# Kernel tuning notes

Hardware: AMD Instinct MI355X
Metric: run time of the kernel (lower is better)

Reference implementation:

```python
import jax, jax.numpy as jnp
import numpy as np

N, E, D, H, L, G, OUT = 16384, 65536, 64, 128, 3, 512, 128
EPS = 1e-5


def setup_inputs() -> dict:
    key = jax.random.key(0)
    ks = jax.random.split(key, 12)
    s = 0.05  # small init to keep res+ stack stable
    return {
        "x": jax.random.normal(ks[0], (N, D), jnp.float32),
        "edge_index": jax.random.randint(ks[1], (2, E), 0, N, jnp.int32),
        "edge_attr": jax.random.normal(ks[2], (E, D), jnp.float32),
        "batch": jnp.sort(jax.random.randint(ks[3], (N,), 0, G, jnp.int32)),
        # per-layer params, stacked on leading layer dim L
        "ln_scale": jnp.ones((L, D), jnp.float32),
        "ln_bias": jnp.zeros((L, D), jnp.float32),
        "W1": jax.random.normal(ks[4], (L, D, H), jnp.float32) * s,
        "b1": jnp.zeros((L, H), jnp.float32),
        "W2": jax.random.normal(ks[5], (L, H, D * D), jnp.float32) * s,
        "b2": jnp.zeros((L, D * D), jnp.float32),
        "root": jax.random.normal(ks[6], (L, D, D), jnp.float32) * s,
        "conv_b": jnp.zeros((L, D), jnp.float32),
        # head params
        "dense_W": jax.random.normal(ks[7], (D, D), jnp.float32) * s,
        "dense_b": jnp.zeros((D,), jnp.float32),
        "out_W": jax.random.normal(ks[8], (D, OUT), jnp.float32) * s,
        "out_b": jnp.zeros((OUT,), jnp.float32),
    }


def _layer_norm(h, scale, bias):
    mu = jnp.mean(h, axis=-1, keepdims=True)
    var = jnp.mean((h - mu) ** 2, axis=-1, keepdims=True)
    return (h - mu) * jax.lax.rsqrt(var + EPS) * scale + bias


def _gnn_layer(x, edge_index, edge_attr, ln_scale, ln_bias, W1, b1, W2, b2, root, conv_b):
    # DeepGCNLayer block='res+': h = conv(dropout(act(norm(x)))); return x + h
    # (dropout is identity in eval/reference)
    h = jax.nn.leaky_relu(_layer_norm(x, ln_scale, ln_bias))
    src, dst = edge_index[0], edge_index[1]
    # NNConv: per-edge DxD weight from edge MLP (MapE2NxN with LeakyReLU)
    w = jax.nn.leaky_relu(edge_attr @ W1 + b1) @ W2 + b2       # [E, D*D]
    w = w.reshape(-1, D, D)                                     # [E, D, D]
    msg = jnp.einsum('ed,edf->ef', h[src], w)                   # [E, D]
    num = jax.ops.segment_sum(msg, dst, num_segments=N)         # [N, D]
    deg = jax.ops.segment_sum(jnp.ones((msg.shape[0],), msg.dtype), dst, num_segments=N)
    agg = num / jnp.maximum(deg, 1.0)[:, None]                  # mean aggregation
    conv = agg + h @ root + conv_b                              # root weight + bias
    return x + conv


def reference(x, edge_index, edge_attr, batch, ln_scale, ln_bias, W1, b1, W2, b2,
              root, conv_b, dense_W, dense_b, out_W, out_b):
    for l in range(L):
        x = _gnn_layer(x, edge_index, edge_attr, ln_scale[l], ln_bias[l],
                       W1[l], b1[l], W2[l], b2[l], root[l], conv_b[l])
    x = x @ dense_W + dense_b
    # global_mean_pool over graphs
    num = jax.ops.segment_sum(x, batch, num_segments=G)
    cnt = jax.ops.segment_sum(jnp.ones((x.shape[0],), x.dtype), batch, num_segments=G)
    pooled = num / jnp.maximum(cnt, 1.0)[:, None]
    pooled = jax.nn.leaky_relu(pooled)
    return pooled @ out_W + out_b
```

## Files before the change

kernel.cpp:

```cpp
#include <hip/hip_runtime.h>
#include <hip/hip_bf16.h>

#define NN 16384
#define EE 65536
#define DD 64
#define HH 128
#define LL 3
#define GG 512
#define OUTD 128
#define NEG 0.01f

#define CHUNK 8192
#define KSEG 8


typedef __attribute__((ext_vector_type(8))) short short8;
typedef __attribute__((ext_vector_type(4))) float f32x4;

__device__ __forceinline__ float leaky(float x){ return x > 0.f ? x : NEG * x; }
__device__ __forceinline__ unsigned short f2bf(float f){
  union { float f; unsigned int u; } v; v.f = f;
  unsigned int r = v.u + 0x7fffu + ((v.u >> 16) & 1u);
  return (unsigned short)(r >> 16);
}

#define CV_A (EE*DD)
#define CV_B (LL*HH*DD)
#define CV_C (LL*64*8192)
#define PRE0 (NN/4)
#define PRE1 ((CV_A+CV_B+CV_C)/256)
#define PRE2 (EE/256)

__global__ void k_pre(const float* x_in, const float* ln_s, const float* ln_b,
                      float* x_cur, float* h, int* deg, int* cursor, int* cnt, float* pooled,
                      const float* ea, const float* W1, const float* W2,
                      unsigned short* eab, unsigned short* W1T, unsigned short* W2T,
                      const int* ei, const int* batch){
  int t = threadIdx.x;
  int b = blockIdx.x;
  if (b < PRE0){
    int i = b*256 + t;
    if (i < NN){ deg[i] = 0; cursor[i] = 0; }
    if (i < GG) cnt[i] = 0;
    if (i < GG*DD) pooled[i] = 0.f;
    int lane = t & 63, nl = t >> 6;
    int n = b*4 + nl;
    float v = x_in[(size_t)n*DD + lane];
    x_cur[(size_t)n*DD + lane] = v;
    float s = v;
    for (int m=1;m<64;m<<=1) s += __shfl_xor(s, m, 64);
    float mu = s * (1.0f/64.0f);
    float dv = v - mu;
    float q = dv*dv;
    for (int m=1;m<64;m<<=1) q += __shfl_xor(q, m, 64);
    float var = q * (1.0f/64.0f);
    float w = dv * rsqrtf(var + 1e-5f) * ln_s[lane] + ln_b[lane];
    h[(size_t)n*DD + lane] = leaky(w);
    return;
  }
  if (b < PRE0 + PRE1){
    int idx = (b - PRE0)*256 + t;
    if (idx < CV_A){
      eab[idx] = f2bf(ea[idx]);
    } else if (idx < CV_A + CV_B){
      int i = idx - CV_A;
      int l = i >> 13, r = i & 8191;
      int j = r >> 6, d = r & 63;
      W1T[i] = f2bf(W1[(size_t)l*DD*HH + d*HH + j]);
    } else {
      int i = idx - CV_A - CV_B;
      int l = i >> 19, rem = i & ((1<<19)-1);
      int f = rem >> 13, c = rem & 8191;
      int kk = c & 1, j = (c>>1) & 3, lane = (c>>3) & 63, ii = (c>>9) & 7, q = (c>>12) & 1;
      int idxu = 2*lane + kk;
      int d = 32*q + 4*ii + j;
      int kd = idxu*64 + d;
      W2T[i] = f2bf(W2[(size_t)l*HH*DD*DD + (size_t)kd*DD + f]);
    }
    return;
  }
  {
    int e = (b - PRE0 - PRE1)*256 + t;
    atomicAdd(&deg[ei[EE + e]], 1);
    if (e < NN) atomicAdd(&cnt[batch[e]], 1);
  }
}

__global__ void k_scan(const int* deg, int* row_ptr){
  __shared__ int part[256];
  int t = threadIdx.x;
  int base = t*64; int s = 0;
  for (int i=0;i<64;++i) s += deg[base+i];
  part[t] = s; __syncthreads();
  for (int off=1; off<256; off<<=1){
    int v = (t>=off)?part[t-off]:0; __syncthreads();
    part[t] += v; __syncthreads();
  }
  int run = (t==0)?0:part[t-1];
  if (t==0) row_ptr[0] = 0;
  for (int i=0;i<64;++i){ run += deg[base+i]; row_ptr[base+i+1] = run; }
}
__global__ void k_fill(const int* ei, const int* row_ptr, int* cursor,
                       int* edge_id, int* src_sorted){
  int e = blockIdx.x*256 + threadIdx.x;
  if (e < EE){
    int d = ei[EE + e];
    int pos = row_ptr[d] + atomicAdd(&cursor[d], 1);
    edge_id[pos] = e;
    src_sorted[pos] = ei[e];
  }
}

__global__ __launch_bounds__(256, 2)
void k_mlp3(const unsigned short* eab, const unsigned short* W1T, const float* b1,
            const int* edge_id, unsigned short* ug){
  __shared__ __align__(16) unsigned short a_lds[128][72];
  __shared__ __align__(16) unsigned short b_lds[128][72];
  __shared__ __align__(16) unsigned short c_lds[128][136];
  int t = threadIdx.x;
  int l  = blockIdx.x >> 9;
  int e0 = (blockIdx.x & 511) * 128;
  {
    int row = t >> 1, col = (t & 1) * 32;
    int eid = edge_id[e0 + row];
    const float4* sa = (const float4*)(eab + (size_t)eid*DD + col);
    const float4* sb = (const float4*)(W1T + (size_t)l*HH*DD + (size_t)row*DD + col);
    #pragma unroll
    for (int i=0;i<4;++i){
      *(float4*)&a_lds[row][col + 8*i] = sa[i];
      *(float4*)&b_lds[row][col + 8*i] = sb[i];
    }
  }
  __syncthreads();
  int wave = t >> 6, lane = t & 63;
  int m0 = (wave >> 1) * 64, j0 = (wave & 1) * 64;
  int lr = lane & 15, lq = lane >> 4;
  f32x4 acc[4][4];
  #pragma unroll
  for (int a=0;a<4;++a)
    #pragma unroll
    for (int b=0;b<4;++b) acc[a][b] = (f32x4){0.f,0.f,0.f,0.f};
  #pragma unroll
  for (int ks=0; ks<2; ++ks){
    short8 av[4];
    #pragma unroll
    for (int mt=0; mt<4; ++mt) av[mt] = *(const short8*)&a_lds[m0 + mt*16 + lr][ks*32 + lq*8];
    #pragma unroll
    for (int jt=0; jt<4; ++jt){
      short8 bv = *(const short8*)&b_lds[j0 + jt*16 + lr][ks*32 + lq*8];
      #pragma unroll
      for (int mt=0; mt<4; ++mt)
        acc[mt][jt] = __builtin_amdgcn_mfma_f32_16x16x32_bf16(av[mt], bv, acc[mt][jt], 0, 0, 0);
    }
  }
  #pragma unroll
  for (int mt=0; mt<4; ++mt)
    #pragma unroll
    for (int jt=0; jt<4; ++jt){
      int col = j0 + jt*16 + lr;
      float bj = b1[l*HH + col];
      #pragma unroll
      for (int r=0; r<4; ++r){
        int row = m0 + mt*16 + lq*4 + r;
        c_lds[row][col] = f2bf(leaky(acc[mt][jt][r] + bj));
      }
    }
  __syncthreads();
  {
    int row = t >> 1, half = t & 1;
    float4* dst = (float4*)(ug + (size_t)l*EE*HH + (size_t)(e0 + row)*HH + half*64);
    #pragma unroll
    for (int i=0;i<8;++i) dst[i] = *(const float4*)&c_lds[row][half*64 + 8*i];
  }
}

__global__ __launch_bounds__(256, 4)
void k_sbuild5(const unsigned short* ug, const float* h, const int* row_ptr,
               const int* src_sorted,
               unsigned short* S, float* Hs, int chunk_base){
  int t = threadIdx.x, wave = t >> 6, lane = t & 63;
  int q = wave & 1;
  int nloc = blockIdx.x*2 + (wave >> 1);
  int n = chunk_base + nloc;
  int r0 = row_ptr[n], r1 = row_ptr[n+1];
  int dbase = 32*q;
  int lhalf = lane & 31;
  const unsigned int* ugd = (const unsigned int*)ug;
  float acc[64];
  #pragma unroll
  for (int i=0;i<64;++i) acc[i] = 0.f;
  float hs = 0.f;
  int pos = r0;
  for (; pos + 4 <= r1; pos += 4){
    int sa0 = src_sorted[pos],   sb0 = src_sorted[pos+1];
    int sa1 = src_sorted[pos+2], sb1 = src_sorted[pos+3];
    int sel0 = (lane < 32) ? sa0 : sb0;
    int sel1 = (lane < 32) ? sa1 : sb1;
    float hv0 = h[(size_t)sel0*DD + dbase + lhalf];
    float hv1 = h[(size_t)sel1*DD + dbase + lhalf];
    unsigned int ua0 = ugd[(size_t)(pos+0)*64 + lane];
    unsigned int ub0 = ugd[(size_t)(pos+1)*64 + lane];
    unsigned int ua1 = ugd[(size_t)(pos+2)*64 + lane];
    unsigned int ub1 = ugd[(size_t)(pos+3)*64 + lane];
    hs += hv0 + hv1;
    int h0 = __float_as_int(hv0), h1 = __float_as_int(hv1);
    float ua0l = __uint_as_float(ua0 << 16), ua0h = __uint_as_float(ua0 & 0xFFFF0000u);
    float ub0l = __uint_as_float(ub0 << 16), ub0h = __uint_as_float(ub0 & 0xFFFF0000u);
    float ua1l = __uint_as_float(ua1 << 16), ua1h = __uint_as_float(ua1 & 0xFFFF0000u);
    float ub1l = __uint_as_float(ub1 << 16), ub1h = __uint_as_float(ub1 & 0xFFFF0000u);
    #pragma unroll
    for (int dd=0; dd<32; ++dd){
      float sa_ = __int_as_float(__builtin_amdgcn_readlane(h0, dd));
      float sb_ = __int_as_float(__builtin_amdgcn_readlane(h0, 32+dd));
      float sa2 = __int_as_float(__builtin_amdgcn_readlane(h1, dd));
      float sb2 = __int_as_float(__builtin_amdgcn_readlane(h1, 32+dd));
      acc[dd*2+0] += ua0l*sa_; acc[dd*2+1] += ua0h*sa_;
      acc[dd*2+0] += ub0l*sb_; acc[dd*2+1] += ub0h*sb_;
      acc[dd*2+0] += ua1l*sa2; acc[dd*2+1] += ua1h*sa2;
      acc[dd*2+0] += ub1l*sb2; acc[dd*2+1] += ub1h*sb2;
    }
  }
  for (; pos + 2 <= r1; pos += 2){
    int sa = src_sorted[pos], sb = src_sorted[pos+1];
    int sel = (lane < 32) ? sa : sb;
    float hv = h[(size_t)sel*DD + dbase + lhalf];
    unsigned int ua = ugd[(size_t)(pos+0)*64 + lane];
    unsigned int ub = ugd[(size_t)(pos+1)*64 + lane];
    hs += hv;
    int h0 = __float_as_int(hv);
    float ual = __uint_as_float(ua << 16), uah = __uint_as_float(ua & 0xFFFF0000u);
    float ubl = __uint_as_float(ub << 16), ubh = __uint_as_float(ub & 0xFFFF0000u);
    #pragma unroll
    for (int dd=0; dd<32; ++dd){
      float sa_ = __int_as_float(__builtin_amdgcn_readlane(h0, dd));
      float sb_ = __int_as_float(__builtin_amdgcn_readlane(h0, 32+dd));
      acc[dd*2+0] += ual*sa_; acc[dd*2+1] += uah*sa_;
      acc[dd*2+0] += ubl*sb_; acc[dd*2+1] += ubh*sb_;
    }
  }
  if (pos < r1){
    int s = src_sorted[pos];
    float hv = h[(size_t)s*DD + dbase + lhalf];
    unsigned int ua = ugd[(size_t)pos*64 + lane];
    hs += (lane < 32) ? hv : 0.f;
    int h0 = __float_as_int(hv);
    float ual = __uint_as_float(ua << 16), uah = __uint_as_float(ua & 0xFFFF0000u);
    #pragma unroll
    for (int dd=0; dd<32; ++dd){
      float sa_ = __int_as_float(__builtin_amdgcn_readlane(h0, dd));
      acc[dd*2+0] += ual*sa_; acc[dd*2+1] += uah*sa_;
    }
  }
  float4* Srow4 = (float4*)(S + (size_t)nloc*8192);
  #pragma unroll
  for (int i=0;i<8;++i){
    union { unsigned int u[4]; float4 v; } b;
    #pragma unroll
    for (int j=0;j<4;++j){
      int dd = 4*i + j;
      b.u[j] = (unsigned int)f2bf(acc[dd*2+0]) | ((unsigned int)f2bf(acc[dd*2+1]) << 16);
    }
    Srow4[(q*8 + i)*64 + lane] = b.v;
  }
  float hs2 = hs + __shfl_xor(hs, 32, 64);
  if (lane < 32) Hs[(size_t)n*DD + dbase + lane] = hs2;
}

__global__ __launch_bounds__(256, 2)
void k_gemm(const unsigned short* S, const unsigned short* W2T,
            float* num_part, int chunk_base){
  __shared__ __align__(16) unsigned short a_lds[128][136];
  __shared__ __align__(16) unsigned short b_lds[64][136];
  int t = threadIdx.x;
  int wave = t >> 6, lane = t & 63;
  int rowblk = blockIdx.x, kseg = blockIdx.y;
  int lr = lane & 15, lq = lane >> 4;
  f32x4 acc[2][4];
  #pragma unroll
  for (int a=0;a<2;++a)
    #pragma unroll
    for (int b=0;b<4;++b) acc[a][b] = (f32x4){0.f,0.f,0.f,0.f};
  int m0 = wave * 32;
  int ra = t >> 1, qa = t & 1;
  int rb = t >> 2, qb = t & 3;
  for (int it = 0; it < 8; ++it){
    int kbase = kseg*1024 + it*128;
    {
      const float4* sa = (const float4*)(S + (size_t)(rowblk*128 + ra)*8192 + kbase + qa*64);
      float4* da = (float4*)&a_lds[ra][qa*64];
      #pragma unroll
      for (int i=0;i<8;++i) da[i] = sa[i];
      const float4* sb = (const float4*)(W2T + (size_t)rb*8192 + kbase + qb*32);
      float4* db = (float4*)&b_lds[rb][qb*32];
      #pragma unroll
      for (int i=0;i<4;++i) db[i] = sb[i];
    }
    __syncthreads();
    #pragma unroll
    for (int kk=0; kk<128; kk+=32){
      short8 a0 = *(const short8*)&a_lds[m0 + lr][kk + lq*8];
      short8 a1 = *(const short8*)&a_lds[m0 + 16 + lr][kk + lq*8];
      #pragma unroll
      for (int ft=0; ft<4; ++ft){
        short8 bv = *(const short8*)&b_lds[ft*16 + lr][kk + lq*8];
        acc[0][ft] = __builtin_amdgcn_mfma_f32_16x16x32_bf16(a0, bv, acc[0][ft], 0, 0, 0);
        acc[1][ft] = __builtin_amdgcn_mfma_f32_16x16x32_bf16(a1, bv, acc[1][ft], 0, 0, 0);
      }
    }
    __syncthreads();
  }
  float* dstp = num_part + (size_t)kseg*NN*DD;
  #pragma unroll
  for (int rt=0; rt<2; ++rt)
    #pragma unroll
    for (int ft=0; ft<4; ++ft)
      #pragma unroll
      for (int rr=0; rr<4; ++rr){
        int m = m0 + rt*16 + lq*4 + rr;
        int f = ft*16 + lr;
        int n = chunk_base + rowblk*128 + m;
        dstp[(size_t)n*DD + f] = acc[rt][ft][rr];
      }
}

__global__ void k_update_ln(float* x, const float* num_part, float* h, const float* Hs,
                            const int* deg, const float* root, const float* b2,
                            const float* conv_b, const float* ln_s, const float* ln_b,
                            int l, int do_ln){
  __shared__ float rl[64][64];
  __shared__ float b2l[64][64];
  __shared__ float hrow[4][64];
  __shared__ float hsrow[4][64];
  int t = threadIdx.x;
  int f = t & 63, nl = t >> 6;
  for (int idx=t; idx<4096; idx+=256){
    rl[idx>>6][idx&63]  = root[(size_t)l*4096 + idx];
    b2l[idx>>6][idx&63] = b2[(size_t)l*4096 + idx];
  }
  int nbase = blockIdx.x*16;
  float cb = conv_b[l*DD + f];
  for (int i=0;i<4;++i){
    int n = nbase + i*4 + nl;
    __syncthreads();
    hrow[nl][f]  = h[(size_t)n*DD + f];
    hsrow[nl][f] = Hs[(size_t)n*DD + f];
    __syncthreads();
    float dg = (float)deg[n]; if (dg < 1.f) dg = 1.f;
    float nsum = 0.f;
    #pragma unroll
    for (int p=0; p<KSEG; ++p) nsum += num_part[(size_t)p*NN*DD + (size_t)n*DD + f];
    float acc = x[(size_t)n*DD + f] + nsum/dg + cb;
    #pragma unroll
    for (int d=0; d<64; ++d)
      acc += hrow[nl][d]*rl[d][f] + hsrow[nl][d]*b2l[d][f];
    x[(size_t)n*DD + f] = acc;
    if (do_ln){
      int lp = l + 1;
      float s = acc;
      for (int m=1;m<64;m<<=1) s += __shfl_xor(s, m, 64);
      float mu = s * (1.0f/64.0f);
      float dv = acc - mu;
      float qv = dv*dv;
      for (int m=1;m<64;m<<=1) qv += __shfl_xor(qv, m, 64);
      float var = qv * (1.0f/64.0f);
      float w = dv * rsqrtf(var + 1e-5f) * ln_s[lp*DD + f] + ln_b[lp*DD + f];
      h[(size_t)n*DD + f] = leaky(w);
    }
  }
}

__global__ void k_dense_pool(const float* x, const float* dW, const float* db,
                             const int* batch, float* pooled){
  __shared__ float wl[64][64];
  __shared__ float xrow[4][64];
  int t = threadIdx.x;
  int f = t & 63, nl = t >> 6;
  for (int idx=t; idx<4096; idx+=256) wl[idx>>6][idx&63] = dW[idx];
  int nbase = blockIdx.x*16;
  float dbf = db[f];
  for (int i=0;i<4;++i){
    int n = nbase + i*4 + nl;
    __syncthreads();
    xrow[nl][f] = x[(size_t)n*DD + f];
    __syncthreads();
    float acc = dbf;
    #pragma unroll
    for (int d=0; d<64; ++d) acc += xrow[nl][d]*wl[d][f];
    atomicAdd(&pooled[(size_t)batch[n]*DD + f], acc);
  }
}

__global__ void k_final(const float* pooled, const int* cnt, const float* oW,
                        const float* ob, float* out){
  __shared__ float p[64];
  int g = blockIdx.x, t = threadIdx.x;
  if (t < 64){
    float c = (float)cnt[g]; if (c < 1.f) c = 1.f;
    p[t] = leaky(pooled[(size_t)g*DD + t] / c);
  }
  __syncthreads();
  float acc = ob[t];
  #pragma unroll
  for (int f=0; f<64; ++f) acc += p[f]*oW[(size_t)f*OUTD + t];
  out[(size_t)g*OUTD + t] = acc;
}

__global__ void k_diag(float* out, float val, int n){
  int i = blockIdx.x*256 + threadIdx.x;
  if (i < n) out[i] = (i==0) ? val : 0.f;
}

extern "C" void kernel_launch(void* const* d_in, const int* in_sizes, int n_in,
                              void* d_out, int out_size, void* d_ws, size_t ws_size,
                              hipStream_t stream){
  const float* x_in  = (const float*)d_in[0];
  const int*   ei    = (const int*)d_in[1];
  const float* ea    = (const float*)d_in[2];
  const int*   batch = (const int*)d_in[3];
  const float* ln_s  = (const float*)d_in[4];
  const float* ln_b  = (const float*)d_in[5];
  const float* W1    = (const float*)d_in[6];
  const float* b1    = (const float*)d_in[7];
  const float* W2    = (const float*)d_in[8];
  const float* b2    = (const float*)d_in[9];
  const float* root  = (const float*)d_in[10];
  const float* convb = (const float*)d_in[11];
  const float* dW    = (const float*)d_in[12];
  const float* db    = (const float*)d_in[13];
  const float* oW    = (const float*)d_in[14];
  const float* ob    = (const float*)d_in[15];
  float* out = (float*)d_out;

  char* ws = (char*)d_ws;
  size_t off = 0;
  auto alloc = [&](size_t bytes)->char*{
    char* p = ws + off; off = (off + bytes + 255) & ~(size_t)255; return p;
  };
  float* x_cur  = (float*)alloc((size_t)NN*DD*4);
  float* h      = (float*)alloc((size_t)NN*DD*4);
  unsigned short* ug  = (unsigned short*)alloc((size_t)LL*EE*HH*2);
  float* num_part = (float*)alloc((size_t)KSEG*NN*DD*4);
  float* Hs     = (float*)alloc((size_t)NN*DD*4);
  unsigned short* S   = (unsigned short*)alloc((size_t)CHUNK*8192*2);
  unsigned short* W2T = (unsigned short*)alloc((size_t)LL*8192*64*2);
  unsigned short* eab = (unsigned short*)alloc((size_t)EE*DD*2);
  unsigned short* W1T = (unsigned short*)alloc((size_t)LL*HH*DD*2);
  int* deg     = (int*)alloc((size_t)NN*4);
  int* row_ptr = (int*)alloc((size_t)(NN+1)*4);
  int* cursor  = (int*)alloc((size_t)NN*4);
  int* edge_id = (int*)alloc((size_t)EE*4);
  int* src_sorted = (int*)alloc((size_t)EE*4);
  int* cnt     = (int*)alloc((size_t)GG*4);
  float* pooled= (float*)alloc((size_t)GG*DD*4);
  size_t needed = off;
  if (ws_size < needed){
    k_diag<<<(out_size+255)/256, 256, 0, stream>>>(out, (float)ws_size, out_size);
    return;
  }

  k_pre <<<PRE0+PRE1+PRE2, 256, 0, stream>>>(x_in, ln_s, ln_b, x_cur, h, deg, cursor, cnt,
                                             pooled, ea, W1, W2, eab, W1T, W2T, ei, batch);
  k_scan<<<1, 256, 0, stream>>>(deg, row_ptr);
  k_fill<<<EE/256, 256, 0, stream>>>(ei, row_ptr, cursor, edge_id, src_sorted);
  k_mlp3<<<LL*(EE/128), 256, 0, stream>>>(eab, W1T, b1, edge_id, ug);

  for (int l=0; l<LL; ++l){
    const unsigned short* ugl = ug + (size_t)l*EE*HH;
    for (int c=0; c<NN/CHUNK; ++c){
      k_sbuild5<<<CHUNK/2, 256, 0, stream>>>(ugl, h, row_ptr, src_sorted, S, Hs, c*CHUNK);
      k_gemm   <<<dim3(CHUNK/128, KSEG), 256, 0, stream>>>(S, W2T + (size_t)l*8192*64, num_part, c*CHUNK);
    }
    k_update_ln<<<NN/16, 256, 0, stream>>>(x_cur, num_part, h, Hs, deg, root, b2, convb,
                                           ln_s, ln_b, l, (l < LL-1) ? 1 : 0);
  }
  k_dense_pool<<<NN/16, 256, 0, stream>>>(x_cur, dW, db, batch, pooled);
  k_final     <<<GG, 128, 0, stream>>>(pooled, cnt, oW, ob, out);
}
```

Baseline: 592.0 us.

## Fuse per-node S construction with W2 GEMM in shared memory

Replaces the two-kernel pipeline (build the per-node S matrix in global memory, then a split-K GEMM writing partial sums) with one fused kernel. Each block of 32 nodes builds K-slices of S in swizzled LDS and immediately multiplies them by W2T with MFMA, accumulating over all K in registers. This removes the large global S buffer and the KSEG partial-sum reduction, and W2T is re-laid out to match. In exchange, each node re-reads its edge gather once per K-slice (8 times), and the grid is smaller with a heavy LDS footprint, which can limit occupancy.

```diff
diff --git a/kernel.cpp b/kernel.cpp
--- a/kernel.cpp
+++ b/kernel.cpp
@@ -9,9 +9,6 @@
 #define GG 512
 #define OUTD 128
 #define NEG 0.01f
-
-#define CHUNK 8192
-#define KSEG 8
 
 
 typedef __attribute__((ext_vector_type(8))) short short8;
@@ -71,11 +68,10 @@
       int i = idx - CV_A - CV_B;
       int l = i >> 19, rem = i & ((1<<19)-1);
       int f = rem >> 13, c = rem & 8191;
-      int kk = c & 1, j = (c>>1) & 3, lane = (c>>3) & 63, ii = (c>>9) & 7, q = (c>>12) & 1;
-      int idxu = 2*lane + kk;
-      int d = 32*q + 4*ii + j;
-      int kd = idxu*64 + d;
-      W2T[i] = f2bf(W2[(size_t)l*HH*DD*DD + (size_t)kd*DD + f]);
+      int ks = c >> 10, cl = c & 1023;
+      int d = cl >> 4, il = cl & 15;
+      int kh = ks*16 + il;
+      W2T[i] = f2bf(W2[(size_t)l*HH*DD*DD + (size_t)kh*DD*DD + (size_t)d*DD + f]);
     }
     return;
   }
@@ -174,156 +170,102 @@
   }
 }
 
-__global__ __launch_bounds__(256, 4)
-void k_sbuild5(const unsigned short* ug, const float* h, const int* row_ptr,
-               const int* src_sorted,
-               unsigned short* S, float* Hs, int chunk_base){
+#define ACC2(w, hv, base) { \
+  float lo_ = __uint_as_float((w) << 16); \
+  float hi_ = __uint_as_float((w) & 0xffff0000u); \
+  acc[(base)]   += lo_*(hv); \
+  acc[(base)+1] += hi_*(hv); }
+
+#define EDGE_ACC(aa, bb, hv) \
+  ACC2((aa).x, hv, 0)  ACC2((aa).y, hv, 2)  ACC2((aa).z, hv, 4)  ACC2((aa).w, hv, 6) \
+  ACC2((bb).x, hv, 8)  ACC2((bb).y, hv,10)  ACC2((bb).z, hv,12)  ACC2((bb).w, hv,14)
+
+__global__ __launch_bounds__(256)
+void k_fused(const unsigned short* ug, const float* h, const int* row_ptr,
+             const int* src_sorted, const unsigned short* W2T,
+             float* num, float* Hs){
+  __shared__ __align__(16) unsigned short Sm[32*1024];
+  char* Sb = (char*)Sm;
   int t = threadIdx.x, wave = t >> 6, lane = t & 63;
-  int q = wave & 1;
-  int nloc = blockIdx.x*2 + (wave >> 1);
-  int n = chunk_base + nloc;
-  int r0 = row_ptr[n], r1 = row_ptr[n+1];
-  int dbase = 32*q;
-  int lhalf = lane & 31;
-  const unsigned int* ugd = (const unsigned int*)ug;
-  float acc[64];
+  int g0 = blockIdx.x * 32;
+  int lr = lane & 15, lq = lane >> 4;
+  int f0 = wave * 16;
+  f32x4 acc0 = (f32x4){0.f,0.f,0.f,0.f};
+  f32x4 acc1 = (f32x4){0.f,0.f,0.f,0.f};
+  int wbase = (wave*8)*2048 + lane*32;
+
+  for (int ks = 0; ks < 8; ++ks){
+    const unsigned short* ugk = ug + ks*16;
+    for (int ni = 0; ni < 8; ++ni){
+      int n = g0 + wave*8 + ni;
+      int r0 = row_ptr[n], r1 = row_ptr[n+1];
+      float acc[16];
+      #pragma unroll
+      for (int i=0;i<16;++i) acc[i] = 0.f;
+      float hs = 0.f;
+      int pos = r0;
+      for (; pos + 4 <= r1; pos += 4){
+        int s0 = src_sorted[pos+0], s1 = src_sorted[pos+1];
+        int s2 = src_sorted[pos+2], s3 = src_sorted[pos+3];
+        const uint4* u0 = (const uint4*)(ugk + (size_t)(pos+0)*HH);
+        const uint4* u1 = (const uint4*)(ugk + (size_t)(pos+1)*HH);
+        const uint4* u2 = (const uint4*)(ugk + (size_t)(pos+2)*HH);
+        const uint4* u3 = (const uint4*)(ugk + (size_t)(pos+3)*HH);
+        float hv0 = h[(size_t)s0*DD + lane];
+        float hv1 = h[(size_t)s1*DD + lane];
+        float hv2 = h[(size_t)s2*DD + lane];
+        float hv3 = h[(size_t)s3*DD + lane];
+        uint4 a0 = u0[0], c0 = u0[1];
+        uint4 a1 = u1[0], c1 = u1[1];
+        uint4 a2 = u2[0], c2 = u2[1];
+        uint4 a3 = u3[0], c3 = u3[1];
+        hs += (hv0 + hv1) + (hv2 + hv3);
+        EDGE_ACC(a0, c0, hv0)
+        EDGE_ACC(a1, c1, hv1)
+        EDGE_ACC(a2, c2, hv2)
+        EDGE_ACC(a3, c3, hv3)
+      }
+      for (; pos < r1; ++pos){
+        int s0 = src_sorted[pos];
+        const uint4* u0 = (const uint4*)(ugk + (size_t)pos*HH);
+        float hv0 = h[(size_t)s0*DD + lane];
+        uint4 a0 = u0[0], c0 = u0[1];
+        hs += hv0;
+        EDGE_ACC(a0, c0, hv0)
+      }
+      unsigned int w[8];
+      #pragma unroll
+      for (int i=0;i<8;++i)
+        w[i] = (unsigned int)f2bf(acc[2*i]) | ((unsigned int)f2bf(acc[2*i+1]) << 16);
+      int nloc = wave*8 + ni;
+      int off = (wbase + ni*2048) ^ ((nloc & 7) << 4);
+      *(float4*)(Sb + off)        = *(const float4*)&w[0];
+      *(float4*)(Sb + (off ^ 16)) = *(const float4*)&w[4];
+      if (ks == 0) Hs[(size_t)n*DD + lane] = hs;
+    }
+    __syncthreads();
+    {
+      const short8* Wp = (const short8*)(W2T + (size_t)(f0 + lr)*8192 + (size_t)ks*1024 + lq*8);
+      #pragma unroll
+      for (int kst = 0; kst < 32; ++kst){
+        short8 bv = Wp[kst*4];
+        int off = ((lr*2048 + lq*16 + kst*64) ^ ((lr&7)<<4));
+        short8 a0 = *(const short8*)(Sb + off);
+        short8 a1 = *(const short8*)(Sb + off + 32768);
+        acc0 = __builtin_amdgcn_mfma_f32_16x16x32_bf16(a0, bv, acc0, 0, 0, 0);
+        acc1 = __builtin_amdgcn_mfma_f32_16x16x32_bf16(a1, bv, acc1, 0, 0, 0);
+      }
+    }
+    __syncthreads();
+  }
   #pragma unroll
-  for (int i=0;i<64;++i) acc[i] = 0.f;
-  float hs = 0.f;
-  int pos = r0;
-  for (; pos + 4 <= r1; pos += 4){
-    int sa0 = src_sorted[pos],   sb0 = src_sorted[pos+1];
-    int sa1 = src_sorted[pos+2], sb1 = src_sorted[pos+3];
-    int sel0 = (lane < 32) ? sa0 : sb0;
-    int sel1 = (lane < 32) ? sa1 : sb1;
-    float hv0 = h[(size_t)sel0*DD + dbase + lhalf];
-    float hv1 = h[(size_t)sel1*DD + dbase + lhalf];
-    unsigned int ua0 = ugd[(size_t)(pos+0)*64 + lane];
-    unsigned int ub0 = ugd[(size_t)(pos+1)*64 + lane];
-    unsigned int ua1 = ugd[(size_t)(pos+2)*64 + lane];
-    unsigned int ub1 = ugd[(size_t)(pos+3)*64 + lane];
-    hs += hv0 + hv1;
-    int h0 = __float_as_int(hv0), h1 = __float_as_int(hv1);
-    float ua0l = __uint_as_float(ua0 << 16), ua0h = __uint_as_float(ua0 & 0xFFFF0000u);
-    float ub0l = __uint_as_float(ub0 << 16), ub0h = __uint_as_float(ub0 & 0xFFFF0000u);
-    float ua1l = __uint_as_float(ua1 << 16), ua1h = __uint_as_float(ua1 & 0xFFFF0000u);
-    float ub1l = __uint_as_float(ub1 << 16), ub1h = __uint_as_float(ub1 & 0xFFFF0000u);
-    #pragma unroll
-    for (int dd=0; dd<32; ++dd){
-      float sa_ = __int_as_float(__builtin_amdgcn_readlane(h0, dd));
-      float sb_ = __int_as_float(__builtin_amdgcn_readlane(h0, 32+dd));
-      float sa2 = __int_as_float(__builtin_amdgcn_readlane(h1, dd));
-      float sb2 = __int_as_float(__builtin_amdgcn_readlane(h1, 32+dd));
-      acc[dd*2+0] += ua0l*sa_; acc[dd*2+1] += ua0h*sa_;
-      acc[dd*2+0] += ub0l*sb_; acc[dd*2+1] += ub0h*sb_;
-      acc[dd*2+0] += ua1l*sa2; acc[dd*2+1] += ua1h*sa2;
-      acc[dd*2+0] += ub1l*sb2; acc[dd*2+1] += ub1h*sb2;
-    }
-  }
-  for (; pos + 2 <= r1; pos += 2){
-    int sa = src_sorted[pos], sb = src_sorted[pos+1];
-    int sel = (lane < 32) ? sa : sb;
-    float hv = h[(size_t)sel*DD + dbase + lhalf];
-    unsigned int ua = ugd[(size_t)(pos+0)*64 + lane];
-    unsigned int ub = ugd[(size_t)(pos+1)*64 + lane];
-    hs += hv;
-    int h0 = __float_as_int(hv);
-    float ual = __uint_as_float(ua << 16), uah = __uint_as_float(ua & 0xFFFF0000u);
-    float ubl = __uint_as_float(ub << 16), ubh = __uint_as_float(ub & 0xFFFF0000u);
-    #pragma unroll
-    for (int dd=0; dd<32; ++dd){
-      float sa_ = __int_as_float(__builtin_amdgcn_readlane(h0, dd));
-      float sb_ = __int_as_float(__builtin_amdgcn_readlane(h0, 32+dd));
-      acc[dd*2+0] += ual*sa_; acc[dd*2+1] += uah*sa_;
-      acc[dd*2+0] += ubl*sb_; acc[dd*2+1] += ubh*sb_;
-    }
-  }
-  if (pos < r1){
-    int s = src_sorted[pos];
-    float hv = h[(size_t)s*DD + dbase + lhalf];
-    unsigned int ua = ugd[(size_t)pos*64 + lane];
-    hs += (lane < 32) ? hv : 0.f;
-    int h0 = __float_as_int(hv);
-    float ual = __uint_as_float(ua << 16), uah = __uint_as_float(ua & 0xFFFF0000u);
-    #pragma unroll
-    for (int dd=0; dd<32; ++dd){
-      float sa_ = __int_as_float(__builtin_amdgcn_readlane(h0, dd));
-      acc[dd*2+0] += ual*sa_; acc[dd*2+1] += uah*sa_;
-    }
-  }
-  float4* Srow4 = (float4*)(S + (size_t)nloc*8192);
-  #pragma unroll
-  for (int i=0;i<8;++i){
-    union { unsigned int u[4]; float4 v; } b;
-    #pragma unroll
-    for (int j=0;j<4;++j){
-      int dd = 4*i + j;
-      b.u[j] = (unsigned int)f2bf(acc[dd*2+0]) | ((unsigned int)f2bf(acc[dd*2+1]) << 16);
-    }
-    Srow4[(q*8 + i)*64 + lane] = b.v;
-  }
-  float hs2 = hs + __shfl_xor(hs, 32, 64);
-  if (lane < 32) Hs[(size_t)n*DD + dbase + lane] = hs2;
-}
-
-__global__ __launch_bounds__(256, 2)
-void k_gemm(const unsigned short* S, const unsigned short* W2T,
-            float* num_part, int chunk_base){
-  __shared__ __align__(16) unsigned short a_lds[128][136];
-  __shared__ __align__(16) unsigned short b_lds[64][136];
-  int t = threadIdx.x;
-  int wave = t >> 6, lane = t & 63;
-  int rowblk = blockIdx.x, kseg = blockIdx.y;
-  int lr = lane & 15, lq = lane >> 4;
-  f32x4 acc[2][4];
-  #pragma unroll
-  for (int a=0;a<2;++a)
-    #pragma unroll
-    for (int b=0;b<4;++b) acc[a][b] = (f32x4){0.f,0.f,0.f,0.f};
-  int m0 = wave * 32;
-  int ra = t >> 1, qa = t & 1;
-  int rb = t >> 2, qb = t & 3;
-  for (int it = 0; it < 8; ++it){
-    int kbase = kseg*1024 + it*128;
-    {
-      const float4* sa = (const float4*)(S + (size_t)(rowblk*128 + ra)*8192 + kbase + qa*64);
-      float4* da = (float4*)&a_lds[ra][qa*64];
-      #pragma unroll
-      for (int i=0;i<8;++i) da[i] = sa[i];
-      const float4* sb = (const float4*)(W2T + (size_t)rb*8192 + kbase + qb*32);
-      float4* db = (float4*)&b_lds[rb][qb*32];
-      #pragma unroll
-      for (int i=0;i<4;++i) db[i] = sb[i];
-    }
-    __syncthreads();
-    #pragma unroll
-    for (int kk=0; kk<128; kk+=32){
-      short8 a0 = *(const short8*)&a_lds[m0 + lr][kk + lq*8];
-      short8 a1 = *(const short8*)&a_lds[m0 + 16 + lr][kk + lq*8];
-      #pragma unroll
-      for (int ft=0; ft<4; ++ft){
-        short8 bv = *(const short8*)&b_lds[ft*16 + lr][kk + lq*8];
-        acc[0][ft] = __builtin_amdgcn_mfma_f32_16x16x32_bf16(a0, bv, acc[0][ft], 0, 0, 0);
-        acc[1][ft] = __builtin_amdgcn_mfma_f32_16x16x32_bf16(a1, bv, acc[1][ft], 0, 0, 0);
-      }
-    }
-    __syncthreads();
-  }
-  float* dstp = num_part + (size_t)kseg*NN*DD;
-  #pragma unroll
-  for (int rt=0; rt<2; ++rt)
-    #pragma unroll
-    for (int ft=0; ft<4; ++ft)
-      #pragma unroll
-      for (int rr=0; rr<4; ++rr){
-        int m = m0 + rt*16 + lq*4 + rr;
-        int f = ft*16 + lr;
-        int n = chunk_base + rowblk*128 + m;
-        dstp[(size_t)n*DD + f] = acc[rt][ft][rr];
-      }
-}
-
-__global__ void k_update_ln(float* x, const float* num_part, float* h, const float* Hs,
+  for (int r=0; r<4; ++r){
+    num[(size_t)(g0      + lq*4 + r)*DD + f0 + lr] = acc0[r];
+    num[(size_t)(g0 + 16 + lq*4 + r)*DD + f0 + lr] = acc1[r];
+  }
+}
+
+__global__ void k_update_ln(float* x, const float* num, float* h, const float* Hs,
                             const int* deg, const float* root, const float* b2,
                             const float* conv_b, const float* ln_s, const float* ln_b,
                             int l, int do_ln){
@@ -346,9 +288,7 @@
     hsrow[nl][f] = Hs[(size_t)n*DD + f];
     __syncthreads();
     float dg = (float)deg[n]; if (dg < 1.f) dg = 1.f;
-    float nsum = 0.f;
-    #pragma unroll
-    for (int p=0; p<KSEG; ++p) nsum += num_part[(size_t)p*NN*DD + (size_t)n*DD + f];
+    float nsum = num[(size_t)n*DD + f];
     float acc = x[(size_t)n*DD + f] + nsum/dg + cb;
     #pragma unroll
     for (int d=0; d<64; ++d)
@@ -439,9 +379,8 @@
   float* x_cur  = (float*)alloc((size_t)NN*DD*4);
   float* h      = (float*)alloc((size_t)NN*DD*4);
   unsigned short* ug  = (unsigned short*)alloc((size_t)LL*EE*HH*2);
-  float* num_part = (float*)alloc((size_t)KSEG*NN*DD*4);
+  float* num    = (float*)alloc((size_t)NN*DD*4);
   float* Hs     = (float*)alloc((size_t)NN*DD*4);
-  unsigned short* S   = (unsigned short*)alloc((size_t)CHUNK*8192*2);
   unsigned short* W2T = (unsigned short*)alloc((size_t)LL*8192*64*2);
   unsigned short* eab = (unsigned short*)alloc((size_t)EE*DD*2);
   unsigned short* W1T = (unsigned short*)alloc((size_t)LL*HH*DD*2);
@@ -465,12 +404,9 @@
   k_mlp3<<<LL*(EE/128), 256, 0, stream>>>(eab, W1T, b1, edge_id, ug);
 
   for (int l=0; l<LL; ++l){
-    const unsigned short* ugl = ug + (size_t)l*EE*HH;
-    for (int c=0; c<NN/CHUNK; ++c){
-      k_sbuild5<<<CHUNK/2, 256, 0, stream>>>(ugl, h, row_ptr, src_sorted, S, Hs, c*CHUNK);
-      k_gemm   <<<dim3(CHUNK/128, KSEG), 256, 0, stream>>>(S, W2T + (size_t)l*8192*64, num_part, c*CHUNK);
-    }
-    k_update_ln<<<NN/16, 256, 0, stream>>>(x_cur, num_part, h, Hs, deg, root, b2, convb,
+    k_fused<<<NN/32, 256, 0, stream>>>(ug + (size_t)l*EE*HH, h, row_ptr, src_sorted,
+                                       W2T + (size_t)l*64*8192, num, Hs);
+    k_update_ln<<<NN/16, 256, 0, stream>>>(x_cur, num, h, Hs, deg, root, b2, convb,
                                            ln_s, ln_b, l, (l < LL-1) ? 1 : 0);
   }
   k_dense_pool<<<NN/16, 256, 0, stream>>>(x_cur, dW, db, batch, pooled);
```

Measured after the change: 746.7 us. +26.1%, slower.
